# Performance work log

Measured on AMD Instinct MI355X. Metric: run time of the kernel, lower is better.

The kernel has to match this reference:

```python
import jax, jax.numpy as jnp
import numpy as np

B, S, D, M = 4, 2048, 1024, 4  # batch, seq_len, d_model, n_stride_masks


def setup_inputs() -> dict:
    key = jax.random.key(0)
    ks = jax.random.split(key, 10)
    lin = lambda k: jax.random.normal(k, (D, D), jnp.float32) / np.float32(np.sqrt(D))
    return {
        "x": jax.random.normal(ks[0], (B, S, D), jnp.float32),
        "stride_masks": jax.random.randint(ks[1], (M, S, S), 0, 2, jnp.int32),
        "Wq": lin(ks[2]), "bq": jnp.zeros((D,), jnp.float32),
        "Wk": lin(ks[3]), "bk": jnp.zeros((D,), jnp.float32),
        "Wv": lin(ks[4]), "bv": jnp.zeros((D,), jnp.float32),
        "Wo": lin(ks[5]), "bo": jnp.zeros((D,), jnp.float32),
    }


def reference(x, stride_masks, Wq, bq, Wk, bk, Wv, bv, Wo, bo):
    scale = jnp.float32(np.sqrt(D))
    Q = x @ Wq + bq  # [B,S,D]
    K = x @ Wk + bk
    V = x @ Wv + bv
    # scores are identical for every mask; compute once (same math as the loop)
    scores = jnp.einsum("bqd,bkd->bqk", Q, K) / scale  # [B,S,S]
    masked = jnp.where(stride_masks[:, None] == 0, jnp.float32(-1e9), scores[None])  # [M,B,S,S]
    weights = jax.nn.softmax(masked, axis=-1)
    # sum over masks then divide by M == mean(stack(outs), 0)
    out = jnp.einsum("mbqk,bkd->bqd", weights, V) / jnp.float32(M)
    return out @ Wo + bo
```

## Files before the change

kernel.cpp:

```cpp
#include <hip/hip_runtime.h>
#include <hip/hip_bf16.h>
#include <stdint.h>

#define B_ 4
#define S_ 2048
#define D_ 1024
#define M_ 4

typedef __bf16 bf16;
typedef _Float16 f16;
typedef unsigned char u8;
typedef __bf16 bf16x8 __attribute__((ext_vector_type(8)));
typedef _Float16 f16x8 __attribute__((ext_vector_type(8)));
typedef float f32x4 __attribute__((ext_vector_type(4)));

__device__ __forceinline__ void async_copy16(const void* g, void* l) {
  __builtin_amdgcn_global_load_lds(
      (const __attribute__((address_space(1))) void*)g,
      (__attribute__((address_space(3))) void*)l, 16, 0, 0);
}

__global__ __launch_bounds__(256) void prep(
    const float* __restrict__ x, const float* __restrict__ w0,
    const float* __restrict__ w1, const float* __restrict__ w2,
    const float* __restrict__ w3, const int* __restrict__ masks,
    bf16* __restrict__ xc, bf16* __restrict__ WT, u8* __restrict__ pk) {
  __shared__ bf16 t[64][65];
  const int blk = blockIdx.x;
  const int tid = threadIdx.x;
  const long SS = (long)S_ * S_;

  if (blk < 4096) {
    const long i = (long)blk * 2048 + tid * 8;
    const float4 a = *(const float4*)(x + i);
    const float4 b = *(const float4*)(x + i + 4);
    bf16x8 o;
    o[0] = (bf16)a.x; o[1] = (bf16)a.y; o[2] = (bf16)a.z; o[3] = (bf16)a.w;
    o[4] = (bf16)b.x; o[5] = (bf16)b.y; o[6] = (bf16)b.z; o[7] = (bf16)b.w;
    *(bf16x8*)(xc + i) = o;
  } else if (blk < 5120) {
    const int local = blk - 4096;
    const int z = local >> 8;
    const int rem = local & 255;
    const int r0 = (rem >> 4) * 64;
    const int c0 = (rem & 15) * 64;
    const int tx = tid & 63;
    const int ty = tid >> 6;
    const float* in = (z == 0) ? w0 : (z == 1) ? w1 : (z == 2) ? w2 : w3;
    bf16* out = WT + (long)z * D_ * D_;
    for (int i = ty; i < 64; i += 4)
      t[i][tx] = (bf16)in[(long)(r0 + i) * D_ + c0 + tx];
    __syncthreads();
    for (int i = ty; i < 64; i += 4)
      out[(long)(c0 + i) * D_ + r0 + tx] = t[tx][i];
  } else {
    const long e = (long)(blk - 5120) * 2048 + tid * 8;
    unsigned long long wv = 0;
#pragma unroll
    for (int m = 0; m < M_; ++m) {
      const int4 a = *(const int4*)(masks + m * SS + e);
      const int4 b = *(const int4*)(masks + m * SS + e + 4);
      const int v[8] = {a.x, a.y, a.z, a.w, b.x, b.y, b.z, b.w};
#pragma unroll
      for (int j = 0; j < 8; ++j)
        wv |= (unsigned long long)(v[j] != 0 ? 1u : 0u) << (8 * j + m);
    }
    *(unsigned long long*)(pk + e) = wv;
  }
}

__global__ __launch_bounds__(256) void transposeB(
    const bf16* __restrict__ in, bf16* __restrict__ out,
    int rows, int cols, long ib, long ob) {
  __shared__ bf16 t[64][65];
  in += (long)blockIdx.z * ib;
  out += (long)blockIdx.z * ob;
  const int r0 = blockIdx.y * 64;
  const int c0 = blockIdx.x * 64;
  const int tx = threadIdx.x & 63;
  const int ty = threadIdx.x >> 6;
#pragma unroll
  for (int i = ty; i < 64; i += 4) t[i][tx] = in[(long)(r0 + i) * cols + c0 + tx];
  __syncthreads();
#pragma unroll
  for (int i = ty; i < 64; i += 4) out[(long)(c0 + i) * rows + r0 + tx] = t[tx][i];
}

#define MODE_PLAIN 0
#define MODE_EXP 1
#define MODE_QKV 2
#define MODE_PV 3

template <typename OutT, int MODE>
__global__ __launch_bounds__(512) void gemmA(
    const bf16* __restrict__ A, int lda,
    const bf16* __restrict__ Bt, long bzs, int ldb,
    OutT* __restrict__ C, int ldc,
    const float* __restrict__ bias0, const float* __restrict__ bias1,
    const float* __restrict__ bias2, float alpha, int K) {
  __shared__ __align__(16) bf16 As[2][2][256 * 32];
  __shared__ __align__(16) bf16 Bs[2][2][128 * 32];
  const int tid = threadIdx.x;
  const int lane = tid & 63;
  const int w = tid >> 6;
  const int wm = w & 3;
  const int wn = w >> 2;
  const int quad = lane >> 4;
  const int l15 = lane & 15;
  const int fse = (quad ^ ((l15 >> 1) & 3)) << 3;

  const int gx = gridDim.x;
  const int pid = blockIdx.y * gx + blockIdx.x;
  const int gsz = 8 * gx;
  const int bym = (pid / gsz) * 8 + (pid % 8);
  const int bxm = (pid % gsz) / 8;
  const int row0 = bym * 256;
  const int col0 = bxm * 128;

  const bf16* Arow = A + (long)row0 * lda;
  const bf16* Bcol;
  int grp = 0;
  if (MODE == MODE_QKV) {
    grp = col0 >> 10;
    Bcol = Bt + (long)grp * ((long)D_ * D_) + (long)(col0 & (D_ - 1)) * ldb;
  } else if (MODE == MODE_PV || MODE == MODE_EXP) {
    Bcol = Bt + (long)(row0 >> 11) * bzs + (long)col0 * ldb;
  } else {
    Bcol = Bt + (long)col0 * ldb;
  }

  const int sr = tid >> 2;
  const int sc = ((tid & 3) ^ ((tid >> 3) & 3)) << 3;
  const bf16* gA = Arow + (long)sr * lda + sc;
  const bf16* gB = Bcol + (long)sr * ldb + sc;
  const int dstoff = (tid >> 6) << 9;
  const long a128 = (long)128 * lda;

#define STAGE(h)                                                       \
  {                                                                    \
    const int kc_ = (h) * 32;                                          \
    bf16* da_ = &As[((h) >> 1) & 1][(h) & 1][0] + dstoff;              \
    bf16* db_ = &Bs[((h) >> 1) & 1][(h) & 1][0] + dstoff;              \
    async_copy16(gA + kc_, da_);                                       \
    async_copy16(gA + kc_ + a128, da_ + 4096);                         \
    async_copy16(gB + kc_, db_);                                       \
  }

#define READF(Ra, Rb, bufv, ksv)                                           \
  {                                                                        \
    const bf16* pa_ = &As[bufv][ksv][0];                                   \
    const bf16* pb_ = &Bs[bufv][ksv][0];                                   \
    _Pragma("unroll") for (int j = 0; j < 4; ++j) {                        \
      Ra[j] = *(const bf16x8*)&pa_[(wm * 64 + j * 16 + l15) * 32 + fse];   \
      Rb[j] = *(const bf16x8*)&pb_[(wn * 64 + j * 16 + l15) * 32 + fse];   \
    }                                                                      \
  }

#define MM(Ra, Rb)                                                         \
  __builtin_amdgcn_s_setprio(1);                                           \
  _Pragma("unroll") for (int mi = 0; mi < 4; ++mi)                         \
      _Pragma("unroll") for (int ni = 0; ni < 4; ++ni) acc[mi][ni] =       \
          __builtin_amdgcn_mfma_f32_16x16x32_bf16(Ra[mi], Rb[ni],          \
                                                  acc[mi][ni], 0, 0, 0);   \
  __builtin_amdgcn_s_setprio(0);

  f32x4 acc[4][4];
#pragma unroll
  for (int i = 0; i < 4; ++i)
#pragma unroll
    for (int j = 0; j < 4; ++j) acc[i][j] = (f32x4){0.f, 0.f, 0.f, 0.f};

  const int nk = K >> 6;

  STAGE(0);
  STAGE(1);
  STAGE(2);
  asm volatile("s_waitcnt vmcnt(6)" ::: "memory");
  __builtin_amdgcn_s_barrier();
  __builtin_amdgcn_sched_barrier(0);

  bf16x8 a0[4], b0[4], a1[4], b1[4];
  READF(a0, b0, 0, 0);

  for (int t = 0; t < nk; ++t) {
    const int buf = t & 1;

    if (t + 1 < nk)
      asm volatile("s_waitcnt vmcnt(3)" ::: "memory");
    else
      asm volatile("s_waitcnt vmcnt(0)" ::: "memory");
    __builtin_amdgcn_s_barrier();
    __builtin_amdgcn_sched_barrier(0);
    READF(a1, b1, buf, 1);
    if (t + 1 < nk) STAGE(2 * t + 3);
    MM(a0, b0);

    if (t + 1 < nk) {
      asm volatile("s_waitcnt vmcnt(3)" ::: "memory");
      __builtin_amdgcn_s_barrier();
      __builtin_amdgcn_sched_barrier(0);
      READF(a0, b0, buf ^ 1, 0);
      if (t + 3 <= nk) STAGE(2 * t + 4);
    }
    MM(a1, b1);
  }

#undef STAGE
#undef READF
#undef MM

  const float* bias = (MODE == MODE_QKV)
                          ? (grp == 0 ? bias0 : grp == 1 ? bias1 : bias2)
                          : bias0;
  const long NX = (long)B_ * S_ * D_;
  OutT* Cb = (MODE == MODE_QKV) ? C + (long)grp * NX : C;
#pragma unroll
  for (int mi = 0; mi < 4; ++mi)
#pragma unroll
    for (int ni = 0; ni < 4; ++ni) {
      const int col = col0 + wn * 64 + ni * 16 + l15;
      const int ccol = (MODE == MODE_QKV) ? (col & (D_ - 1)) : col;
      const float bv = bias ? bias[ccol] : 0.0f;
#pragma unroll
      for (int r = 0; r < 4; ++r) {
        const int row = row0 + wm * 64 + mi * 16 + quad * 4 + r;
        const float val = acc[mi][ni][r] * alpha + bv;
        if (MODE == MODE_EXP) {
          Cb[(long)row * ldc + col] = (OutT)__expf(val);
        } else if (MODE == MODE_QKV) {
          Cb[(long)row * D_ + ccol] = (OutT)val;
        } else {
          Cb[(long)row * ldc + col] = (OutT)val;
        }
      }
    }
}

__global__ __launch_bounds__(256) void softmax_combine(
    const f16* __restrict__ E, const u8* __restrict__ pk, bf16* __restrict__ P) {
  const int q = blockIdx.x;
  const int b = blockIdx.y;
  const int tid = threadIdx.x;
  const int lane = tid & 63;
  const int wv = tid >> 6;
  __shared__ float4 red[4];

  float e[8];
  {
    const f16x8 h = *(const f16x8*)(E + ((long)b * S_ + q) * S_ + tid * 8);
#pragma unroll
    for (int j = 0; j < 8; ++j) e[j] = (float)h[j];
  }
  const unsigned long long mb =
      *(const unsigned long long*)(pk + (long)q * S_ + tid * 8);

  float4 s = {0.f, 0.f, 0.f, 0.f};
#pragma unroll
  for (int j = 0; j < 8; ++j) {
    const unsigned bits = (unsigned)(mb >> (8 * j)) & 0xF;
    const float ev = e[j];
    if (bits & 1) s.x += ev;
    if (bits & 2) s.y += ev;
    if (bits & 4) s.z += ev;
    if (bits & 8) s.w += ev;
  }
#pragma unroll
  for (int o = 32; o > 0; o >>= 1) {
    s.x += __shfl_xor(s.x, o, 64);
    s.y += __shfl_xor(s.y, o, 64);
    s.z += __shfl_xor(s.z, o, 64);
    s.w += __shfl_xor(s.w, o, 64);
  }
  if (lane == 0) red[wv] = s;
  __syncthreads();
  const float4 t0 = red[0], t1 = red[1], t2 = red[2], t3 = red[3];
  const float r0 = 0.25f / (t0.x + t1.x + t2.x + t3.x);
  const float r1 = 0.25f / (t0.y + t1.y + t2.y + t3.y);
  const float r2 = 0.25f / (t0.z + t1.z + t2.z + t3.z);
  const float r3 = 0.25f / (t0.w + t1.w + t2.w + t3.w);

  bf16x8 o;
#pragma unroll
  for (int j = 0; j < 8; ++j) {
    const unsigned bits = (unsigned)(mb >> (8 * j)) & 0xF;
    const float wgt = ((bits & 1) ? r0 : 0.f) + ((bits & 2) ? r1 : 0.f) +
                      ((bits & 4) ? r2 : 0.f) + ((bits & 8) ? r3 : 0.f);
    o[j] = (bf16)(e[j] * wgt);
  }
  *(bf16x8*)(P + ((long)b * S_ + q) * S_ + tid * 8) = o;
}

extern "C" void kernel_launch(void* const* d_in, const int* in_sizes, int n_in,
                              void* d_out, int out_size, void* d_ws, size_t ws_size,
                              hipStream_t stream) {
  const float* x = (const float*)d_in[0];
  const int* masks = (const int*)d_in[1];
  const float* bq = (const float*)d_in[3];
  const float* bk = (const float*)d_in[5];
  const float* bv = (const float*)d_in[7];
  const float* bo = (const float*)d_in[9];
  float* out = (float*)d_out;

  const long DD = (long)D_ * D_;
  const long SD = (long)S_ * D_;
  const long NX = (long)B_ * SD;
  const long SS = (long)S_ * S_;

  bf16* xc = (bf16*)d_ws;
  bf16* WqT = xc + NX;
  bf16* WoT = WqT + 3 * DD;
  u8* pk = (u8*)(WoT + DD);
  bf16* Q = (bf16*)(pk + SS);
  bf16* K = Q + NX;
  bf16* V = K + NX;
  bf16* VT = V + NX;
  bf16* P = VT + NX;
  f16* E = (f16*)(P + (long)B_ * SS);
  bf16* attn = Q;

  dim3 blk(256);
  dim3 blk512(512);

  prep<<<dim3(7168), blk, 0, stream>>>(
      x, (const float*)d_in[2], (const float*)d_in[4], (const float*)d_in[6],
      (const float*)d_in[8], masks, xc, WqT, pk);

  gemmA<bf16, MODE_QKV><<<dim3(24, 32), blk512, 0, stream>>>(
      xc, D_, WqT, 0, D_, Q, D_, bq, bk, bv, 1.0f, D_);

  transposeB<<<dim3(16, 32, B_), blk, 0, stream>>>(V, VT, S_, D_, SD, SD);

  gemmA<f16, MODE_EXP><<<dim3(16, 32), blk512, 0, stream>>>(
      Q, D_, K, SD, D_, E, S_, nullptr, nullptr, nullptr, 1.0f / 32.0f, D_);

  softmax_combine<<<dim3(S_, B_), blk, 0, stream>>>(E, pk, P);

  gemmA<bf16, MODE_PV><<<dim3(8, 32), blk512, 0, stream>>>(
      P, S_, VT, SD, S_, attn, D_, nullptr, nullptr, nullptr, 1.0f, S_);

  gemmA<float, MODE_PLAIN><<<dim3(8, 32), blk512, 0, stream>>>(
      attn, D_, WoT, 0, D_, out, D_, bo, nullptr, nullptr, 1.0f, D_);
}
```

Baseline: 365.8 us.

## Replace four-buffer double-register GEMM pipeline with three-slot ring buffer

Restructures the GEMM main loop from a 2x2 LDS buffer scheme with two register fragment sets into a 3-slot ring of half-K stages, prefetching two stages ahead with one barrier per 32-wide K step. This cuts shared memory from 4 to 3 stage slots, which may raise occupancy, and simplifies the loop. In exchange it loses the register-level double buffering that overlapped LDS reads with MFMA, so LDS latency may become exposed.

```diff
diff --git a/kernel.cpp b/kernel.cpp
--- a/kernel.cpp
+++ b/kernel.cpp
@@ -98,8 +98,8 @@
     OutT* __restrict__ C, int ldc,
     const float* __restrict__ bias0, const float* __restrict__ bias1,
     const float* __restrict__ bias2, float alpha, int K) {
-  __shared__ __align__(16) bf16 As[2][2][256 * 32];
-  __shared__ __align__(16) bf16 Bs[2][2][128 * 32];
+  __shared__ __align__(16) bf16 As[3][256 * 32];
+  __shared__ __align__(16) bf16 Bs[3][128 * 32];
   const int tid = threadIdx.x;
   const int lane = tid & 63;
   const int w = tid >> 6;
@@ -136,20 +136,20 @@
   const int dstoff = (tid >> 6) << 9;
   const long a128 = (long)128 * lda;
 
-#define STAGE(h)                                                       \
+#define STAGE(h, s)                                                    \
   {                                                                    \
     const int kc_ = (h) * 32;                                          \
-    bf16* da_ = &As[((h) >> 1) & 1][(h) & 1][0] + dstoff;              \
-    bf16* db_ = &Bs[((h) >> 1) & 1][(h) & 1][0] + dstoff;              \
+    bf16* da_ = &As[0][0] + (s) * (256 * 32) + dstoff;                 \
+    bf16* db_ = &Bs[0][0] + (s) * (128 * 32) + dstoff;                 \
     async_copy16(gA + kc_, da_);                                       \
     async_copy16(gA + kc_ + a128, da_ + 4096);                         \
     async_copy16(gB + kc_, db_);                                       \
   }
 
-#define READF(Ra, Rb, bufv, ksv)                                           \
+#define READF(Ra, Rb, s)                                                   \
   {                                                                        \
-    const bf16* pa_ = &As[bufv][ksv][0];                                   \
-    const bf16* pb_ = &Bs[bufv][ksv][0];                                   \
+    const bf16* pa_ = &As[0][0] + (s) * (256 * 32);                        \
+    const bf16* pb_ = &Bs[0][0] + (s) * (128 * 32);                        \
     _Pragma("unroll") for (int j = 0; j < 4; ++j) {                        \
       Ra[j] = *(const bf16x8*)&pa_[(wm * 64 + j * 16 + l15) * 32 + fse];   \
       Rb[j] = *(const bf16x8*)&pb_[(wn * 64 + j * 16 + l15) * 32 + fse];   \
@@ -170,39 +170,32 @@
 #pragma unroll
     for (int j = 0; j < 4; ++j) acc[i][j] = (f32x4){0.f, 0.f, 0.f, 0.f};
 
-  const int nk = K >> 6;
-
-  STAGE(0);
-  STAGE(1);
-  STAGE(2);
-  asm volatile("s_waitcnt vmcnt(6)" ::: "memory");
+  const int nh = (K >> 6) << 1;
+
+  STAGE(0, 0);
+  STAGE(1, 1);
+  asm volatile("s_waitcnt vmcnt(3)" ::: "memory");
   __builtin_amdgcn_s_barrier();
   __builtin_amdgcn_sched_barrier(0);
 
-  bf16x8 a0[4], b0[4], a1[4], b1[4];
-  READF(a0, b0, 0, 0);
-
-  for (int t = 0; t < nk; ++t) {
-    const int buf = t & 1;
-
-    if (t + 1 < nk)
+  int s0 = 0;
+  for (int h = 0; h < nh; ++h) {
+    bf16x8 af[4], bf[4];
+    READF(af, bf, s0);
+    if (h + 2 < nh) {
+      const int s2 = (s0 >= 1) ? (s0 - 1) : 2;
+      STAGE(h + 2, s2);
+    }
+    MM(af, bf);
+    if (h + 2 < nh)
       asm volatile("s_waitcnt vmcnt(3)" ::: "memory");
-    else
+    else if (h + 1 < nh)
       asm volatile("s_waitcnt vmcnt(0)" ::: "memory");
-    __builtin_amdgcn_s_barrier();
-    __builtin_amdgcn_sched_barrier(0);
-    READF(a1, b1, buf, 1);
-    if (t + 1 < nk) STAGE(2 * t + 3);
-    MM(a0, b0);
-
-    if (t + 1 < nk) {
-      asm volatile("s_waitcnt vmcnt(3)" ::: "memory");
+    if (h + 1 < nh) {
       __builtin_amdgcn_s_barrier();
       __builtin_amdgcn_sched_barrier(0);
-      READF(a0, b0, buf ^ 1, 0);
-      if (t + 3 <= nk) STAGE(2 * t + 4);
     }
-    MM(a1, b1);
+    s0 = (s0 == 2) ? 0 : (s0 + 1);
   }
 
 #undef STAGE
```

Result: faster. 348.4 us, median of 2 (-4.8%).
